# Kernel optimization log

Hardware: AMD Instinct MI355X
Metric: run time of the kernel (lower is better)

The kernel has to match this reference:

```python
import jax, jax.numpy as jnp
import numpy as np

B, H, W, C = 4, 64, 64, 64
DK = C // 8  # key/query channels from Conv2D(filters=channels//8)


def setup_inputs() -> dict:
    key = jax.random.key(0)
    ks = jax.random.split(key, 4)
    x = jax.random.normal(ks[0], (B, H, W, C), dtype=jnp.float32)
    # he_normal-ish scale for 1x1 conv kernels (fan_in = C)
    s = np.sqrt(2.0 / C).astype(np.float32)
    Wf = jax.random.normal(ks[1], (C, DK), dtype=jnp.float32) * s
    Wg = jax.random.normal(ks[2], (C, DK), dtype=jnp.float32) * s
    Wh = jax.random.normal(ks[3], (C, C), dtype=jnp.float32) * s
    bf = jnp.zeros((DK,), dtype=jnp.float32)
    bg = jnp.zeros((DK,), dtype=jnp.float32)
    bh = jnp.zeros((C,), dtype=jnp.float32)
    return {"x": x, "Wf": Wf, "bf": bf, "Wg": Wg, "bg": bg, "Wh": Wh, "bh": bh}


def reference(x, Wf, bf, Wg, bg, Wh, bh):
    b, h, w, c = x.shape
    n = h * w
    xf = x.reshape(b, n, c)  # 1x1 conv == per-position linear over flattened spatial dims
    f = xf @ Wf + bf         # [B, N, DK]
    g = xf @ Wg + bg         # [B, N, DK]
    v = xf @ Wh + bh         # [B, N, C]
    # attention = softmax(g @ f^T) over keys (tf.nn.softmax default: last axis)
    scores = jnp.einsum('bnd,bmd->bnm', g, f)   # [B, N, N]
    attn = jax.nn.softmax(scores, axis=-1)
    out = jnp.einsum('bnm,bmc->bnc', attn, v)   # [B, N, C]
    return out
```

## Files before the change

kernel.cpp:

```cpp
#include <hip/hip_runtime.h>
#include <hip/hip_bf16.h>
#include <hip/hip_fp16.h>

typedef _Float16 half8_t  __attribute__((ext_vector_type(8)));
typedef short    short8_t __attribute__((ext_vector_type(8)));
typedef float    f32x4    __attribute__((ext_vector_type(4)));

#define LOG2E 1.44269504088896f

__global__ __launch_bounds__(256) void prep_kernel(
    const float* __restrict__ x,
    const float* __restrict__ Wf, const float* __restrict__ bf,
    const float* __restrict__ Wg, const float* __restrict__ bg,
    const float* __restrict__ Wh, const float* __restrict__ bh,
    _Float16* __restrict__ fh, _Float16* __restrict__ gh,
    unsigned short* __restrict__ vT)
{
  __shared__ float XsT[64 * 33];
  __shared__ float Wall[64 * 80];
  __shared__ float ball[80];
  const int t  = threadIdx.x;
  const int p0 = blockIdx.x * 32;

  for (int i = t; i < 512; i += 256) {
    Wall[(i >> 3) * 80 + (i & 7)]     = Wf[i];
    Wall[(i >> 3) * 80 + 8 + (i & 7)] = Wg[i] * LOG2E;
  }
  for (int i = t; i < 4096; i += 256)
    Wall[(i >> 6) * 80 + 16 + (i & 63)] = Wh[i];
  if (t < 80) ball[t] = (t < 8) ? bf[t] : (t < 16) ? bg[t - 8] * LOG2E : bh[t - 16];

  const float4* xs = (const float4*)(x + (size_t)p0 * 64);
#pragma unroll
  for (int i = 0; i < 2; i++) {
    int idx = t + i * 256;
    int row = idx >> 4, c4 = idx & 15;
    float4 v = xs[idx];
    XsT[(c4 * 4 + 0) * 33 + row] = v.x;
    XsT[(c4 * 4 + 1) * 33 + row] = v.y;
    XsT[(c4 * 4 + 2) * 33 + row] = v.z;
    XsT[(c4 * 4 + 3) * 33 + row] = v.w;
  }
  __syncthreads();

  const int pos = t & 31;
  const int g   = t >> 5;
  const int cb  = g * 10;

  float acc[10];
#pragma unroll
  for (int j = 0; j < 10; j++) acc[j] = ball[cb + j];

  for (int c = 0; c < 64; c++) {
    float xv = XsT[c * 33 + pos];
    const float2* wr = (const float2*)&Wall[c * 80 + cb];
#pragma unroll
    for (int k = 0; k < 5; k++) {
      float2 w2 = wr[k];
      acc[2 * k]     += xv * w2.x;
      acc[2 * k + 1] += xv * w2.y;
    }
  }

  const size_t pg = (size_t)p0 + pos;
  const int b = (int)(pg >> 12);
  const int n = (int)(pg & 4095);
  const size_t vidx = (((size_t)b * 128 + (n >> 5)) * 4 + ((n >> 3) & 3)) * 512 + (n & 7);
#pragma unroll
  for (int j = 0; j < 10; j++) {
    int ch = cb + j;
    if (ch < 8) {
      fh[pg * 8 + ch] = (_Float16)acc[j];
    } else if (ch < 16) {
      gh[pg * 8 + (ch - 8)] = (_Float16)acc[j];
    } else {
      __hip_bfloat16 hv = __float2bfloat16(acc[j]);
      vT[vidx + (size_t)(ch - 16) * 8] = *(unsigned short*)&hv;
    }
  }
}

__device__ __forceinline__ unsigned pack_bf16_2(float lo, float hi) {
  float2 f2; f2.x = lo; f2.y = hi;
  __hip_bfloat162 h2 = __float22bfloat162_rn(f2);
  return *reinterpret_cast<unsigned*>(&h2);
}

__global__ __launch_bounds__(512, 4) void attn_kernel(
    const _Float16* __restrict__ fh,
    const _Float16* __restrict__ gh,
    const unsigned short* __restrict__ vT,
    float* __restrict__ out)
{
  const int N    = 4096;
  const int lane = threadIdx.x & 63;
  const int w    = threadIdx.x >> 6;
  const int quad = lane >> 4;
  const int l15  = lane & 15;

  __shared__ float red[7][64][21];

  const int xcd = blockIdx.x & 7;
  const int b   = xcd >> 1;
  const int sub = ((blockIdx.x >> 3) << 1) + (xcd & 1);
  const int q0  = sub * 16;
  const int kbase = w * 512;

  const _Float16* fbase = fh + (size_t)b * N * 8;
  const _Float16* gbase = gh + (size_t)b * N * 8;
  const short*    vbat  = (const short*)vT + (size_t)b * 262144 + (quad << 9) + (l15 << 3);

  half8_t gfrag = {};
  if (quad == 0) gfrag = *(const half8_t*)(gbase + (size_t)(q0 + l15) * 8);

  const f32x4 zc = {0.f, 0.f, 0.f, 0.f};
  f32x4 acc[4] = {zc, zc, zc, zc};
  f32x4 acc4   = zc;

  short8_t ones8;
#pragma unroll
  for (int i = 0; i < 8; i++) ones8[i] = (short)0x3F80;

  const int  srcA = ((quad & 1) << 5) + l15;
  const int  srcB = srcA + 16;
  const bool hi   = (quad >= 2);

  half8_t f0 = {}, f1 = {};

#pragma unroll 8
  for (int cc = 0; cc < 16; cc++) {
    const int k0 = kbase + cc * 32;

    if (quad == 0) {
      f0 = *(const half8_t*)(fbase + (size_t)(k0 + l15) * 8);
      f1 = *(const half8_t*)(fbase + (size_t)(k0 + 16 + l15) * 8);
    }
    const short* vk = vbat + ((size_t)(k0 >> 5) << 11);
    short8_t v0 = *(const short8_t*)(vk);
    short8_t v1 = *(const short8_t*)(vk + 128);
    short8_t v2 = *(const short8_t*)(vk + 256);
    short8_t v3 = *(const short8_t*)(vk + 384);

    f32x4 s0 = __builtin_amdgcn_mfma_f32_16x16x32_f16(f0, gfrag, zc, 0, 0, 0);
    f32x4 s1 = __builtin_amdgcn_mfma_f32_16x16x32_f16(f1, gfrag, zc, 0, 0, 0);

    float p00 = __builtin_amdgcn_exp2f(s0[0]), p01 = __builtin_amdgcn_exp2f(s0[1]);
    float p02 = __builtin_amdgcn_exp2f(s0[2]), p03 = __builtin_amdgcn_exp2f(s0[3]);
    float p10 = __builtin_amdgcn_exp2f(s1[0]), p11 = __builtin_amdgcn_exp2f(s1[1]);
    float p12 = __builtin_amdgcn_exp2f(s1[2]), p13 = __builtin_amdgcn_exp2f(s1[3]);

    unsigned pk00 = pack_bf16_2(p00, p01), pk01 = pack_bf16_2(p02, p03);
    unsigned pk10 = pack_bf16_2(p10, p11), pk11 = pack_bf16_2(p12, p13);

    unsigned t0aA = __shfl((int)pk00, srcA), t0bA = __shfl((int)pk01, srcA);
    unsigned t1aA = __shfl((int)pk10, srcA), t1bA = __shfl((int)pk11, srcA);
    unsigned t0aB = __shfl((int)pk00, srcB), t0bB = __shfl((int)pk01, srcB);
    unsigned t1aB = __shfl((int)pk10, srcB), t1bB = __shfl((int)pk11, srcB);
    union { unsigned u[4]; short8_t v; } au;
    au.u[0] = hi ? t1aA : t0aA;
    au.u[1] = hi ? t1bA : t0bA;
    au.u[2] = hi ? t1aB : t0aB;
    au.u[3] = hi ? t1bB : t0bB;
    short8_t afrag = au.v;

    acc[0] = __builtin_amdgcn_mfma_f32_16x16x32_bf16(afrag, v0, acc[0], 0, 0, 0);
    acc[1] = __builtin_amdgcn_mfma_f32_16x16x32_bf16(afrag, v1, acc[1], 0, 0, 0);
    acc[2] = __builtin_amdgcn_mfma_f32_16x16x32_bf16(afrag, v2, acc[2], 0, 0, 0);
    acc[3] = __builtin_amdgcn_mfma_f32_16x16x32_bf16(afrag, v3, acc[3], 0, 0, 0);
    acc4   = __builtin_amdgcn_mfma_f32_16x16x32_bf16(afrag, ones8, acc4, 0, 0, 0);
  }

  if (w > 0) {
    float* p = &red[w - 1][lane][0];
#pragma unroll
    for (int ct = 0; ct < 4; ct++)
#pragma unroll
      for (int reg = 0; reg < 4; reg++) p[ct * 4 + reg] = acc[ct][reg];
#pragma unroll
    for (int reg = 0; reg < 4; reg++) p[16 + reg] = acc4[reg];
  }
  __syncthreads();
  if (w == 0) {
#pragma unroll
    for (int ww = 0; ww < 7; ww++) {
      const float* p = &red[ww][lane][0];
#pragma unroll
      for (int ct = 0; ct < 4; ct++)
#pragma unroll
        for (int reg = 0; reg < 4; reg++) acc[ct][reg] += p[ct * 4 + reg];
#pragma unroll
      for (int reg = 0; reg < 4; reg++) acc4[reg] += p[16 + reg];
    }
    float inv[4];
#pragma unroll
    for (int reg = 0; reg < 4; reg++) inv[reg] = 1.0f / acc4[reg];

    float* ob = out + ((size_t)b * N + q0) * 64 + l15;
#pragma unroll
    for (int reg = 0; reg < 4; reg++)
#pragma unroll
      for (int ct = 0; ct < 4; ct++)
        ob[(quad * 4 + reg) * 64 + ct * 16] = acc[ct][reg] * inv[reg];
  }
}

extern "C" void kernel_launch(void* const* d_in, const int* in_sizes, int n_in,
                              void* d_out, int out_size, void* d_ws, size_t ws_size,
                              hipStream_t stream) {
  const float* x  = (const float*)d_in[0];
  const float* Wf = (const float*)d_in[1];
  const float* bf = (const float*)d_in[2];
  const float* Wg = (const float*)d_in[3];
  const float* bg = (const float*)d_in[4];
  const float* Wh = (const float*)d_in[5];
  const float* bh = (const float*)d_in[6];
  float* out = (float*)d_out;

  char* ws = (char*)d_ws;
  _Float16* fh = (_Float16*)ws;
  _Float16* gh = (_Float16*)(ws + 262144);
  unsigned short* vT = (unsigned short*)(ws + 524288);

  prep_kernel<<<512, 256, 0, stream>>>(x, Wf, bf, Wg, bg, Wh, bh, fh, gh, vT);
  attn_kernel<<<1024, 512, 0, stream>>>(fh, gh, vT, out);
}
```

Before: 105.5 us.

## Transpose PV MFMA operands to remove cross-lane shuffles and vectorize output stores

Computes the PV product with V as the A operand and P as the B operand, so the exp'd score registers feed the MFMA directly and the per-iteration ds_bpermute shuffles and selects go away. The prep kernel now writes f in a permuted key-slot order and V in a new transposed tile layout so the operands match. The row-sum reduction keeps a single scalar, the LDS reduction buffer shrinks, and the output is written with float4 stores. Launch bounds are raised to 6 waves per SIMD, which may constrain register allocation.

Measured after the change: 120.9 us. +14.5%, slower.

```diff
diff --git a/kernel.cpp b/kernel.cpp
--- a/kernel.cpp
+++ b/kernel.cpp
@@ -65,17 +65,22 @@
   const size_t pg = (size_t)p0 + pos;
   const int b = (int)(pg >> 12);
   const int n = (int)(pg & 4095);
-  const size_t vidx = (((size_t)b * 128 + (n >> 5)) * 4 + ((n >> 3) & 3)) * 512 + (n & 7);
-#pragma unroll
-  for (int j = 0; j < 10; j++) {
-    int ch = cb + j;
+  const int kblock = n >> 5;
+  const int r  = n & 31;
+  const int q8 = r >> 3, j8 = r & 7;
+  const int slot = (j8 < 4) ? (q8 * 4 + j8) : (16 + q8 * 4 + (j8 - 4));
+  const size_t fpos = ((size_t)b * 4096 + (kblock << 5) + slot) * 8;
+  const size_t vbase = (((size_t)b * 128 + kblock) << 11) + r;
+#pragma unroll
+  for (int jj = 0; jj < 10; jj++) {
+    int ch = cb + jj;
     if (ch < 8) {
-      fh[pg * 8 + ch] = (_Float16)acc[j];
+      fh[fpos + ch] = (_Float16)acc[jj];
     } else if (ch < 16) {
-      gh[pg * 8 + (ch - 8)] = (_Float16)acc[j];
+      gh[pg * 8 + (ch - 8)] = (_Float16)acc[jj];
     } else {
-      __hip_bfloat16 hv = __float2bfloat16(acc[j]);
-      vT[vidx + (size_t)(ch - 16) * 8] = *(unsigned short*)&hv;
+      __hip_bfloat16 hv = __float2bfloat16(acc[jj]);
+      vT[vbase + (size_t)(ch - 16) * 32] = *(unsigned short*)&hv;
     }
   }
 }
@@ -86,7 +91,7 @@
   return *reinterpret_cast<unsigned*>(&h2);
 }
 
-__global__ __launch_bounds__(512, 4) void attn_kernel(
+__global__ __launch_bounds__(512, 6) void attn_kernel(
     const _Float16* __restrict__ fh,
     const _Float16* __restrict__ gh,
     const unsigned short* __restrict__ vT,
@@ -98,7 +103,7 @@
   const int quad = lane >> 4;
   const int l15  = lane & 15;
 
-  __shared__ float red[7][64][21];
+  __shared__ float red[7][64][17];
 
   const int xcd = blockIdx.x & 7;
   const int b   = xcd >> 1;
@@ -108,7 +113,7 @@
 
   const _Float16* fbase = fh + (size_t)b * N * 8;
   const _Float16* gbase = gh + (size_t)b * N * 8;
-  const short*    vbat  = (const short*)vT + (size_t)b * 262144 + (quad << 9) + (l15 << 3);
+  const short* vbat = (const short*)vT + (size_t)b * 262144 + (l15 << 5) + (quad << 3);
 
   half8_t gfrag = {};
   if (quad == 0) gfrag = *(const half8_t*)(gbase + (size_t)(q0 + l15) * 8);
@@ -121,10 +126,6 @@
 #pragma unroll
   for (int i = 0; i < 8; i++) ones8[i] = (short)0x3F80;
 
-  const int  srcA = ((quad & 1) << 5) + l15;
-  const int  srcB = srcA + 16;
-  const bool hi   = (quad >= 2);
-
   half8_t f0 = {}, f1 = {};
 
 #pragma unroll 8
@@ -137,9 +138,9 @@
     }
     const short* vk = vbat + ((size_t)(k0 >> 5) << 11);
     short8_t v0 = *(const short8_t*)(vk);
-    short8_t v1 = *(const short8_t*)(vk + 128);
-    short8_t v2 = *(const short8_t*)(vk + 256);
-    short8_t v3 = *(const short8_t*)(vk + 384);
+    short8_t v1 = *(const short8_t*)(vk + 512);
+    short8_t v2 = *(const short8_t*)(vk + 1024);
+    short8_t v3 = *(const short8_t*)(vk + 1536);
 
     f32x4 s0 = __builtin_amdgcn_mfma_f32_16x16x32_f16(f0, gfrag, zc, 0, 0, 0);
     f32x4 s1 = __builtin_amdgcn_mfma_f32_16x16x32_f16(f1, gfrag, zc, 0, 0, 0);
@@ -149,26 +150,21 @@
     float p10 = __builtin_amdgcn_exp2f(s1[0]), p11 = __builtin_amdgcn_exp2f(s1[1]);
     float p12 = __builtin_amdgcn_exp2f(s1[2]), p13 = __builtin_amdgcn_exp2f(s1[3]);
 
-    unsigned pk00 = pack_bf16_2(p00, p01), pk01 = pack_bf16_2(p02, p03);
-    unsigned pk10 = pack_bf16_2(p10, p11), pk11 = pack_bf16_2(p12, p13);
-
-    unsigned t0aA = __shfl((int)pk00, srcA), t0bA = __shfl((int)pk01, srcA);
-    unsigned t1aA = __shfl((int)pk10, srcA), t1bA = __shfl((int)pk11, srcA);
-    unsigned t0aB = __shfl((int)pk00, srcB), t0bB = __shfl((int)pk01, srcB);
-    unsigned t1aB = __shfl((int)pk10, srcB), t1bB = __shfl((int)pk11, srcB);
-    union { unsigned u[4]; short8_t v; } au;
-    au.u[0] = hi ? t1aA : t0aA;
-    au.u[1] = hi ? t1bA : t0bA;
-    au.u[2] = hi ? t1aB : t0aB;
-    au.u[3] = hi ? t1bB : t0bB;
-    short8_t afrag = au.v;
-
-    acc[0] = __builtin_amdgcn_mfma_f32_16x16x32_bf16(afrag, v0, acc[0], 0, 0, 0);
-    acc[1] = __builtin_amdgcn_mfma_f32_16x16x32_bf16(afrag, v1, acc[1], 0, 0, 0);
-    acc[2] = __builtin_amdgcn_mfma_f32_16x16x32_bf16(afrag, v2, acc[2], 0, 0, 0);
-    acc[3] = __builtin_amdgcn_mfma_f32_16x16x32_bf16(afrag, v3, acc[3], 0, 0, 0);
-    acc4   = __builtin_amdgcn_mfma_f32_16x16x32_bf16(afrag, ones8, acc4, 0, 0, 0);
-  }
+    union { unsigned u[4]; short8_t v; } pu;
+    pu.u[0] = pack_bf16_2(p00, p01);
+    pu.u[1] = pack_bf16_2(p02, p03);
+    pu.u[2] = pack_bf16_2(p10, p11);
+    pu.u[3] = pack_bf16_2(p12, p13);
+    short8_t pfrag = pu.v;
+
+    acc[0] = __builtin_amdgcn_mfma_f32_16x16x32_bf16(v0, pfrag, acc[0], 0, 0, 0);
+    acc[1] = __builtin_amdgcn_mfma_f32_16x16x32_bf16(v1, pfrag, acc[1], 0, 0, 0);
+    acc[2] = __builtin_amdgcn_mfma_f32_16x16x32_bf16(v2, pfrag, acc[2], 0, 0, 0);
+    acc[3] = __builtin_amdgcn_mfma_f32_16x16x32_bf16(v3, pfrag, acc[3], 0, 0, 0);
+    acc4   = __builtin_amdgcn_mfma_f32_16x16x32_bf16(ones8, pfrag, acc4, 0, 0, 0);
+  }
+
+  float lv = acc4[0];
 
   if (w > 0) {
     float* p = &red[w - 1][lane][0];
@@ -176,8 +172,7 @@
     for (int ct = 0; ct < 4; ct++)
 #pragma unroll
       for (int reg = 0; reg < 4; reg++) p[ct * 4 + reg] = acc[ct][reg];
-#pragma unroll
-    for (int reg = 0; reg < 4; reg++) p[16 + reg] = acc4[reg];
+    p[16] = lv;
   }
   __syncthreads();
   if (w == 0) {
@@ -188,19 +183,15 @@
       for (int ct = 0; ct < 4; ct++)
 #pragma unroll
         for (int reg = 0; reg < 4; reg++) acc[ct][reg] += p[ct * 4 + reg];
-#pragma unroll
-      for (int reg = 0; reg < 4; reg++) acc4[reg] += p[16 + reg];
-    }
-    float inv[4];
-#pragma unroll
-    for (int reg = 0; reg < 4; reg++) inv[reg] = 1.0f / acc4[reg];
-
-    float* ob = out + ((size_t)b * N + q0) * 64 + l15;
-#pragma unroll
-    for (int reg = 0; reg < 4; reg++)
-#pragma unroll
-      for (int ct = 0; ct < 4; ct++)
-        ob[(quad * 4 + reg) * 64 + ct * 16] = acc[ct][reg] * inv[reg];
+      lv += p[16];
+    }
+    const float inv = 1.0f / lv;
+    float* ob = out + ((size_t)b * N + q0 + l15) * 64 + (quad << 2);
+#pragma unroll
+    for (int ct = 0; ct < 4; ct++) {
+      f32x4 rr = acc[ct] * inv;
+      *(f32x4*)(ob + ct * 16) = rr;
+    }
   }
 }
 
```
